# Kernel tuning notes

Hardware: AMD Instinct MI355X
Metric: run time of the kernel (lower is better)

The kernel has to match this reference:

```python
import jax, jax.numpy as jnp
import numpy as np

N_NODES = 100000
EPS = 1e-12  # F.normalize eps


def _sage_conv(x, src, dst, deg, Wl, bl, Wr):
    # mean aggregation of neighbor (source) features at destination nodes
    agg = jax.ops.segment_sum(x[src], dst, num_segments=N_NODES)  # [N, F]
    agg = agg / jnp.maximum(deg, 1.0)[:, None]
    out = agg @ Wl + bl + x @ Wr  # lin_l(mean(x_j)) + lin_r(x_i)
    # normalize=True -> L2 row normalization
    norm = jnp.sqrt(jnp.sum(out * out, axis=-1, keepdims=True))
    return out / jnp.maximum(norm, EPS)


def setup_inputs() -> dict:
    key = jax.random.key(0)
    ks = jax.random.split(key, 10)
    F_IN, H, C = 14, 32, 2
    x = jax.random.normal(ks[0], (N_NODES, F_IN), dtype=jnp.float32)
    edge_index = jax.random.randint(ks[1], (2, 6400000), 0, N_NODES, dtype=jnp.int32)
    def glorot(k, shape):
        lim = float(np.sqrt(6.0 / (shape[0] + shape[1])))
        return jax.random.uniform(k, shape, jnp.float32, -lim, lim)
    return {
        "x": x,
        "edge_index": edge_index,
        "W1l": glorot(ks[2], (F_IN, H)), "b1": jnp.zeros((H,), jnp.float32),
        "W1r": glorot(ks[3], (F_IN, H)),
        "W2l": glorot(ks[4], (H, H)), "b2": jnp.zeros((H,), jnp.float32),
        "W2r": glorot(ks[5], (H, H)),
        "Wlin": glorot(ks[6], (H, C)), "blin": jnp.zeros((C,), jnp.float32),
    }


def reference(x, edge_index, W1l, b1, W1r, W2l, b2, W2r, Wlin, blin):
    src, dst = edge_index[0], edge_index[1]
    deg = jax.ops.segment_sum(jnp.ones_like(dst, dtype=x.dtype), dst,
                              num_segments=N_NODES)  # in-degree per node
    h = jax.nn.relu(_sage_conv(x, src, dst, deg, W1l, b1, W1r))
    # dropout p=0.2 is identity at inference
    h = jax.nn.relu(_sage_conv(h, src, dst, deg, W2l, b2, W2r))
    return h @ Wlin + blin  # [N, num_classes]
```

## Files before the change

kernel.cpp:

```cpp
#include <hip/hip_runtime.h>
#include <hip/hip_bf16.h>


#define CHA 16384
#define MAXBH 800
#define CAPH 9728
#define NPB 128

static __device__ __forceinline__ unsigned short f2bf(float f) {
    unsigned u = __float_as_uint(f);
    unsigned r = (u + 0x7FFFu + ((u >> 16) & 1u)) >> 16;
    return (unsigned short)r;
}
#define BF_LO(u) __uint_as_float((u) << 16)
#define BF_HI(u) __uint_as_float((u) & 0xFFFF0000u)

__global__ void cvt_x_bf16(const float* __restrict__ x, unsigned short* __restrict__ xb,
                           int* __restrict__ bcursor, int N, int NBH) {
    int idx = blockIdx.x * blockDim.x + threadIdx.x;
    if (idx < NBH) bcursor[idx] = idx * CAPH;
    if (idx >= N * 16) return;
    int n = idx >> 4, f = idx & 15;
    float v = (f < 14) ? x[n * 14 + f] : 0.f;
    xb[idx] = f2bf(v);
}

__global__ __launch_bounds__(1024) void partitionA(
        const int* __restrict__ src, const int* __restrict__ dst,
        int* __restrict__ bcursor, unsigned* __restrict__ part, int E, int NBH) {
    __shared__ unsigned pk[CHA];
    __shared__ int h[MAXBH], lofs[MAXBH], delta[MAXBH];
    int t = threadIdx.x;
    int base = blockIdx.x * CHA;
    int end = base + CHA; if (end > E) end = E;
    int cnt = end - base;

    int ed[16], es[16], er[16];
    for (int i = t; i < NBH; i += 1024) h[i] = 0;
    __syncthreads();
    #pragma unroll
    for (int i = 0; i < 4; ++i) {
        int j = i * 4096 + t * 4;
        if (j + 4 <= cnt) {
            int4 d4 = *(const int4*)(dst + base + j);
            int4 s4 = *(const int4*)(src + base + j);
            ed[i*4+0] = d4.x; ed[i*4+1] = d4.y; ed[i*4+2] = d4.z; ed[i*4+3] = d4.w;
            es[i*4+0] = s4.x; es[i*4+1] = s4.y; es[i*4+2] = s4.z; es[i*4+3] = s4.w;
            er[i*4+0] = atomicAdd(&h[d4.x >> 7], 1);
            er[i*4+1] = atomicAdd(&h[d4.y >> 7], 1);
            er[i*4+2] = atomicAdd(&h[d4.z >> 7], 1);
            er[i*4+3] = atomicAdd(&h[d4.w >> 7], 1);
        } else {
            #pragma unroll
            for (int k = 0; k < 4; ++k) {
                if (j + k < cnt) {
                    ed[i*4+k] = dst[base + j + k];
                    es[i*4+k] = src[base + j + k];
                    er[i*4+k] = atomicAdd(&h[ed[i*4+k] >> 7], 1);
                } else ed[i*4+k] = -1;
            }
        }
    }
    __syncthreads();
    if (t < 64) {
        int vals[13];
        int run = 0;
        int b13 = t * 13;
        #pragma unroll
        for (int i = 0; i < 13; ++i) {
            int idx = b13 + i;
            int x = (idx < NBH) ? h[idx] : 0;
            run += x;
            vals[i] = run;
        }
        int tot = run, sc = run;
        #pragma unroll
        for (int off = 1; off < 64; off <<= 1) {
            int nv = __shfl_up(sc, off);
            if (t >= off) sc += nv;
        }
        int excl = sc - tot;
        #pragma unroll
        for (int i = 0; i < 13; ++i) {
            int idx = b13 + i;
            if (idx < NBH) {
                h[idx] = excl + vals[i];
                lofs[idx] = excl + (i ? vals[i - 1] : 0);
            }
        }
    }
    __syncthreads();
    if (t < NBH) {
        int excl = lofs[t];
        int v = h[t] - excl;
        int g = v ? atomicAdd(&bcursor[t], v) : 0;
        delta[t] = g - excl;
    }
    __syncthreads();
    #pragma unroll
    for (int i = 0; i < 16; ++i) {
        int d = ed[i];
        if (d >= 0) {
            int b = d >> 7;
            pk[lofs[b] + er[i]] = ((unsigned)(d & 127) << 24) | (unsigned)es[i];
        }
    }
    __syncthreads();
    int wid = t >> 6, lane = t & 63;
    for (int b = wid; b < NBH; b += 16) {
        int s = lofs[b];
        int e2 = h[b];
        int dlt = delta[b];
        int lim = (b + 1) * CAPH;
        for (int k = s + lane; k < e2; k += 64) {
            int gidx = dlt + k;
            if (gidx < lim) part[gidx] = pk[k];
        }
    }
}

__global__ __launch_bounds__(1024) void partitionB_fused(
        const unsigned* __restrict__ part, const int* __restrict__ bcursor,
        const uint4* __restrict__ xb4, const float* __restrict__ x,
        const float* __restrict__ W1l, const float* __restrict__ b1,
        const float* __restrict__ W1r,
        int* __restrict__ deg, int* __restrict__ offs, int* __restrict__ nlo,
        int* __restrict__ sorted_src, float* __restrict__ hbuf,
        unsigned short* __restrict__ hb, int N, int HALF) {
    __shared__ int pk2[CAPH];
    __shared__ int hh[256], keyofs[256];
    __shared__ int lstart[128], ldeg[128];
    __shared__ float sagg[128 * 17];
    __shared__ float sx[128 * 14];
    __shared__ float swl[448], swr[448], sb1[32];
    __shared__ int sTot;
    int hbid = blockIdx.x;
    int t = threadIdx.x;
    int start = hbid * CAPH;
    int end = bcursor[hbid];
    if (end > start + CAPH) end = start + CAPH;
    int cnt = end - start;
    unsigned ce[10];
    int rk[10];
    if (t < 256) hh[t] = 0;
    if (t >= 512 && t < 960) { swl[t - 512] = W1l[t - 512]; swr[t - 512] = W1r[t - 512]; }
    else if (t >= 960 && t < 992) sb1[t - 960] = b1[t - 960];
    __syncthreads();
    #pragma unroll
    for (int i = 0; i < 10; ++i) {
        int idx = start + t + i * 1024;
        unsigned p = 0xFFFFFFFFu;
        int r = 0;
        if (idx < end) {
            p = part[idx];
            int key = (int)(p >> 24) * 2 + (((int)(p & 0xFFFFFFu) < HALF) ? 0 : 1);
            r = atomicAdd(&hh[key], 1);
        }
        ce[i] = p;
        rk[i] = r;
    }
    {
        int nbase = hbid * 128;
        int nnod = N - nbase; if (nnod > 128) nnod = 128; if (nnod < 0) nnod = 0;
        const float* gx = x + (size_t)nbase * 14;
        for (int i = t; i < nnod * 14; i += 1024) sx[i] = gx[i];
    }
    __syncthreads();
    if (t < 64) {
        int b4 = t * 4;
        int v0 = hh[b4], v1 = hh[b4 + 1], v2 = hh[b4 + 2], v3 = hh[b4 + 3];
        int s1 = v0 + v1, s2 = s1 + v2, s3 = s2 + v3;
        int sc = s3;
        #pragma unroll
        for (int off = 1; off < 64; off <<= 1) {
            int nv = __shfl_up(sc, off);
            if (t >= off) sc += nv;
        }
        int excl = sc - s3;
        keyofs[b4]     = excl;
        keyofs[b4 + 1] = excl + v0;
        keyofs[b4 + 2] = excl + s1;
        keyofs[b4 + 3] = excl + s2;
        if (t == 63) sTot = excl + s3;
    }
    __syncthreads();
    if (t < 128) {
        int lo = hh[2 * t];
        int d = lo + hh[2 * t + 1];
        int excl = keyofs[2 * t];
        lstart[t] = excl;
        ldeg[t] = d;
        int node = hbid * 128 + t;
        if (node < N) {
            deg[node] = d;
            offs[node] = start + excl;
            nlo[node] = lo;
        }
    }
    __syncthreads();
    #pragma unroll
    for (int i = 0; i < 10; ++i) {
        unsigned p = ce[i];
        if (p != 0xFFFFFFFFu) {
            int s = (int)(p & 0xFFFFFFu);
            int key = (int)(p >> 24) * 2 + ((s < HALF) ? 0 : 1);
            int pos = keyofs[key] + rk[i];
            if (pos < CAPH) pk2[pos] = s;
        }
    }
    __syncthreads();
    int tot = sTot; if (tot > CAPH) tot = CAPH;
    for (int i = t; i < tot; i += 1024)
        sorted_src[start + i] = pk2[i];

    int node = t >> 3, sub = t & 7, ep = sub >> 1, half = sub & 1;
    int js = lstart[node], d = ldeg[node];
    int je = js + d;
    float a[8] = {0,0,0,0,0,0,0,0};
    int j = js + ep;
    for (; j + 12 < je; j += 16) {
        int s0 = pk2[j], s1 = pk2[j + 4], s2 = pk2[j + 8], s3 = pk2[j + 12];
        uint4 u0 = xb4[s0 * 2 + half], u1 = xb4[s1 * 2 + half];
        uint4 u2 = xb4[s2 * 2 + half], u3 = xb4[s3 * 2 + half];
        a[0] += (BF_LO(u0.x) + BF_LO(u1.x)) + (BF_LO(u2.x) + BF_LO(u3.x));
        a[1] += (BF_HI(u0.x) + BF_HI(u1.x)) + (BF_HI(u2.x) + BF_HI(u3.x));
        a[2] += (BF_LO(u0.y) + BF_LO(u1.y)) + (BF_LO(u2.y) + BF_LO(u3.y));
        a[3] += (BF_HI(u0.y) + BF_HI(u1.y)) + (BF_HI(u2.y) + BF_HI(u3.y));
        a[4] += (BF_LO(u0.z) + BF_LO(u1.z)) + (BF_LO(u2.z) + BF_LO(u3.z));
        a[5] += (BF_HI(u0.z) + BF_HI(u1.z)) + (BF_HI(u2.z) + BF_HI(u3.z));
        a[6] += (BF_LO(u0.w) + BF_LO(u1.w)) + (BF_LO(u2.w) + BF_LO(u3.w));
        a[7] += (BF_HI(u0.w) + BF_HI(u1.w)) + (BF_HI(u2.w) + BF_HI(u3.w));
    }
    for (; j + 4 < je; j += 8) {
        int s0 = pk2[j], s1 = pk2[j + 4];
        uint4 u0 = xb4[s0 * 2 + half], u1 = xb4[s1 * 2 + half];
        a[0] += BF_LO(u0.x) + BF_LO(u1.x);
        a[1] += BF_HI(u0.x) + BF_HI(u1.x);
        a[2] += BF_LO(u0.y) + BF_LO(u1.y);
        a[3] += BF_HI(u0.y) + BF_HI(u1.y);
        a[4] += BF_LO(u0.z) + BF_LO(u1.z);
        a[5] += BF_HI(u0.z) + BF_HI(u1.z);
        a[6] += BF_LO(u0.w) + BF_LO(u1.w);
        a[7] += BF_HI(u0.w) + BF_HI(u1.w);
    }
    for (; j < je; j += 4) {
        uint4 u0 = xb4[pk2[j] * 2 + half];
        a[0] += BF_LO(u0.x); a[1] += BF_HI(u0.x);
        a[2] += BF_LO(u0.y); a[3] += BF_HI(u0.y);
        a[4] += BF_LO(u0.z); a[5] += BF_HI(u0.z);
        a[6] += BF_LO(u0.w); a[7] += BF_HI(u0.w);
    }
    #pragma unroll
    for (int i = 0; i < 8; ++i) {
        a[i] += __shfl_xor(a[i], 2);
        a[i] += __shfl_xor(a[i], 4);
    }
    if (ep == 0) {
        #pragma unroll
        for (int i = 0; i < 8; ++i) sagg[node * 17 + half * 8 + i] = a[i];
    }
    __syncthreads();

    float inv = 1.0f / ((d > 0) ? (float)d : 1.0f);
    float acc[4];
    #pragma unroll
    for (int i = 0; i < 4; ++i) acc[i] = sb1[sub * 4 + i];
    #pragma unroll
    for (int k = 0; k < 14; ++k) {
        float ag = sagg[node * 17 + k] * inv;
        float xv = sx[node * 14 + k];
        float4 wl = *(const float4*)&swl[k * 32 + sub * 4];
        float4 wr = *(const float4*)&swr[k * 32 + sub * 4];
        acc[0] += ag * wl.x + xv * wr.x;
        acc[1] += ag * wl.y + xv * wr.y;
        acc[2] += ag * wl.z + xv * wr.z;
        acc[3] += ag * wl.w + xv * wr.w;
    }
    float ss = 0.f;
    #pragma unroll
    for (int i = 0; i < 4; ++i) ss += acc[i] * acc[i];
    ss += __shfl_xor(ss, 1); ss += __shfl_xor(ss, 2); ss += __shfl_xor(ss, 4);
    float invn = 1.f / fmaxf(sqrtf(ss), 1e-12f);
    int gnode = hbid * 128 + node;
    if (gnode < N) {
        float hv[4];
        #pragma unroll
        for (int i = 0; i < 4; ++i) hv[i] = fmaxf(acc[i] * invn, 0.f);
        *(float4*)(hbuf + (size_t)gnode * 32 + sub * 4) =
            make_float4(hv[0], hv[1], hv[2], hv[3]);
        uint2 pb;
        pb.x = (unsigned)f2bf(hv[0]) | ((unsigned)f2bf(hv[1]) << 16);
        pb.y = (unsigned)f2bf(hv[2]) | ((unsigned)f2bf(hv[3]) << 16);
        *(uint2*)(hb + (size_t)gnode * 32 + sub * 4) = pb;
    }
}

__global__ __launch_bounds__(256) void gather32_p0(
        const uint4* __restrict__ hb, const int* __restrict__ sorted_src,
        const int* __restrict__ offs, const int* __restrict__ nlo,
        float4* __restrict__ agg2a, int N) {
    int idx = blockIdx.x * blockDim.x + threadIdx.x;
    int n = idx >> 2;
    if (n >= N) return;
    int q = idx & 3;
    int start = offs[n];
    int jend = nlo[n];
    float a0=0,a1=0,a2=0,a3=0,a4=0,a5=0,a6=0,a7=0;
    int j = 0;
    for (; j + 8 <= jend; j += 8) {
        int s0 = sorted_src[start + j + 0];
        int s1 = sorted_src[start + j + 1];
        int s2 = sorted_src[start + j + 2];
        int s3 = sorted_src[start + j + 3];
        int s4 = sorted_src[start + j + 4];
        int s5 = sorted_src[start + j + 5];
        int s6 = sorted_src[start + j + 6];
        int s7 = sorted_src[start + j + 7];
        uint4 u0 = hb[s0 * 4 + q];
        uint4 u1 = hb[s1 * 4 + q];
        uint4 u2 = hb[s2 * 4 + q];
        uint4 u3 = hb[s3 * 4 + q];
        uint4 u4 = hb[s4 * 4 + q];
        uint4 u5 = hb[s5 * 4 + q];
        uint4 u6 = hb[s6 * 4 + q];
        uint4 u7 = hb[s7 * 4 + q];
        a0 += (BF_LO(u0.x)+BF_LO(u1.x)+BF_LO(u2.x)+BF_LO(u3.x))
            + (BF_LO(u4.x)+BF_LO(u5.x)+BF_LO(u6.x)+BF_LO(u7.x));
        a1 += (BF_HI(u0.x)+BF_HI(u1.x)+BF_HI(u2.x)+BF_HI(u3.x))
            + (BF_HI(u4.x)+BF_HI(u5.x)+BF_HI(u6.x)+BF_HI(u7.x));
        a2 += (BF_LO(u0.y)+BF_LO(u1.y)+BF_LO(u2.y)+BF_LO(u3.y))
            + (BF_LO(u4.y)+BF_LO(u5.y)+BF_LO(u6.y)+BF_LO(u7.y));
        a3 += (BF_HI(u0.y)+BF_HI(u1.y)+BF_HI(u2.y)+BF_HI(u3.y))
            + (BF_HI(u4.y)+BF_HI(u5.y)+BF_HI(u6.y)+BF_HI(u7.y));
        a4 += (BF_LO(u0.z)+BF_LO(u1.z)+BF_LO(u2.z)+BF_LO(u3.z))
            + (BF_LO(u4.z)+BF_LO(u5.z)+BF_LO(u6.z)+BF_LO(u7.z));
        a5 += (BF_HI(u0.z)+BF_HI(u1.z)+BF_HI(u2.z)+BF_HI(u3.z))
            + (BF_HI(u4.z)+BF_HI(u5.z)+BF_HI(u6.z)+BF_HI(u7.z));
        a6 += (BF_LO(u0.w)+BF_LO(u1.w)+BF_LO(u2.w)+BF_LO(u3.w))
            + (BF_LO(u4.w)+BF_LO(u5.w)+BF_LO(u6.w)+BF_LO(u7.w));
        a7 += (BF_HI(u0.w)+BF_HI(u1.w)+BF_HI(u2.w)+BF_HI(u3.w))
            + (BF_HI(u4.w)+BF_HI(u5.w)+BF_HI(u6.w)+BF_HI(u7.w));
    }
    for (; j + 4 <= jend; j += 4) {
        int s0 = sorted_src[start + j + 0];
        int s1 = sorted_src[start + j + 1];
        int s2 = sorted_src[start + j + 2];
        int s3 = sorted_src[start + j + 3];
        uint4 u0 = hb[s0 * 4 + q];
        uint4 u1 = hb[s1 * 4 + q];
        uint4 u2 = hb[s2 * 4 + q];
        uint4 u3 = hb[s3 * 4 + q];
        a0 += BF_LO(u0.x)+BF_LO(u1.x)+BF_LO(u2.x)+BF_LO(u3.x);
        a1 += BF_HI(u0.x)+BF_HI(u1.x)+BF_HI(u2.x)+BF_HI(u3.x);
        a2 += BF_LO(u0.y)+BF_LO(u1.y)+BF_LO(u2.y)+BF_LO(u3.y);
        a3 += BF_HI(u0.y)+BF_HI(u1.y)+BF_HI(u2.y)+BF_HI(u3.y);
        a4 += BF_LO(u0.z)+BF_LO(u1.z)+BF_LO(u2.z)+BF_LO(u3.z);
        a5 += BF_HI(u0.z)+BF_HI(u1.z)+BF_HI(u2.z)+BF_HI(u3.z);
        a6 += BF_LO(u0.w)+BF_LO(u1.w)+BF_LO(u2.w)+BF_LO(u3.w);
        a7 += BF_HI(u0.w)+BF_HI(u1.w)+BF_HI(u2.w)+BF_HI(u3.w);
    }
    for (; j < jend; ++j) {
        uint4 u0 = hb[sorted_src[start + j] * 4 + q];
        a0 += BF_LO(u0.x); a1 += BF_HI(u0.x);
        a2 += BF_LO(u0.y); a3 += BF_HI(u0.y);
        a4 += BF_LO(u0.z); a5 += BF_HI(u0.z);
        a6 += BF_LO(u0.w); a7 += BF_HI(u0.w);
    }
    agg2a[n * 8 + q * 2 + 0] = make_float4(a0, a1, a2, a3);
    agg2a[n * 8 + q * 2 + 1] = make_float4(a4, a5, a6, a7);
}

__global__ __launch_bounds__(256) void gather32_p1(
        const uint4* __restrict__ hb, const int* __restrict__ sorted_src,
        const int* __restrict__ offs, const int* __restrict__ deg,
        const int* __restrict__ nlo, float4* __restrict__ agg2b, int N) {
    int idx = blockIdx.x * blockDim.x + threadIdx.x;
    int n = idx >> 2;
    if (n >= N) return;
    int q = idx & 3;
    int start = offs[n];
    int d = deg[n];
    int j = nlo[n];
    float a0=0,a1=0,a2=0,a3=0,a4=0,a5=0,a6=0,a7=0;
    for (; j + 8 <= d; j += 8) {
        int s0 = sorted_src[start + j + 0];
        int s1 = sorted_src[start + j + 1];
        int s2 = sorted_src[start + j + 2];
        int s3 = sorted_src[start + j + 3];
        int s4 = sorted_src[start + j + 4];
        int s5 = sorted_src[start + j + 5];
        int s6 = sorted_src[start + j + 6];
        int s7 = sorted_src[start + j + 7];
        uint4 u0 = hb[s0 * 4 + q];
        uint4 u1 = hb[s1 * 4 + q];
        uint4 u2 = hb[s2 * 4 + q];
        uint4 u3 = hb[s3 * 4 + q];
        uint4 u4 = hb[s4 * 4 + q];
        uint4 u5 = hb[s5 * 4 + q];
        uint4 u6 = hb[s6 * 4 + q];
        uint4 u7 = hb[s7 * 4 + q];
        a0 += (BF_LO(u0.x)+BF_LO(u1.x)+BF_LO(u2.x)+BF_LO(u3.x))
            + (BF_LO(u4.x)+BF_LO(u5.x)+BF_LO(u6.x)+BF_LO(u7.x));
        a1 += (BF_HI(u0.x)+BF_HI(u1.x)+BF_HI(u2.x)+BF_HI(u3.x))
            + (BF_HI(u4.x)+BF_HI(u5.x)+BF_HI(u6.x)+BF_HI(u7.x));
        a2 += (BF_LO(u0.y)+BF_LO(u1.y)+BF_LO(u2.y)+BF_LO(u3.y))
            + (BF_LO(u4.y)+BF_LO(u5.y)+BF_LO(u6.y)+BF_LO(u7.y));
        a3 += (BF_HI(u0.y)+BF_HI(u1.y)+BF_HI(u2.y)+BF_HI(u3.y))
            + (BF_HI(u4.y)+BF_HI(u5.y)+BF_HI(u6.y)+BF_HI(u7.y));
        a4 += (BF_LO(u0.z)+BF_LO(u1.z)+BF_LO(u2.z)+BF_LO(u3.z))
            + (BF_LO(u4.z)+BF_LO(u5.z)+BF_LO(u6.z)+BF_LO(u7.z));
        a5 += (BF_HI(u0.z)+BF_HI(u1.z)+BF_HI(u2.z)+BF_HI(u3.z))
            + (BF_HI(u4.z)+BF_HI(u5.z)+BF_HI(u6.z)+BF_HI(u7.z));
        a6 += (BF_LO(u0.w)+BF_LO(u1.w)+BF_LO(u2.w)+BF_LO(u3.w))
            + (BF_LO(u4.w)+BF_LO(u5.w)+BF_LO(u6.w)+BF_LO(u7.w));
        a7 += (BF_HI(u0.w)+BF_HI(u1.w)+BF_HI(u2.w)+BF_HI(u3.w))
            + (BF_HI(u4.w)+BF_HI(u5.w)+BF_HI(u6.w)+BF_HI(u7.w));
    }
    for (; j + 4 <= d; j += 4) {
        int s0 = sorted_src[start + j + 0];
        int s1 = sorted_src[start + j + 1];
        int s2 = sorted_src[start + j + 2];
        int s3 = sorted_src[start + j + 3];
        uint4 u0 = hb[s0 * 4 + q];
        uint4 u1 = hb[s1 * 4 + q];
        uint4 u2 = hb[s2 * 4 + q];
        uint4 u3 = hb[s3 * 4 + q];
        a0 += BF_LO(u0.x)+BF_LO(u1.x)+BF_LO(u2.x)+BF_LO(u3.x);
        a1 += BF_HI(u0.x)+BF_HI(u1.x)+BF_HI(u2.x)+BF_HI(u3.x);
        a2 += BF_LO(u0.y)+BF_LO(u1.y)+BF_LO(u2.y)+BF_LO(u3.y);
        a3 += BF_HI(u0.y)+BF_HI(u1.y)+BF_HI(u2.y)+BF_HI(u3.y);
        a4 += BF_LO(u0.z)+BF_LO(u1.z)+BF_LO(u2.z)+BF_LO(u3.z);
        a5 += BF_HI(u0.z)+BF_HI(u1.z)+BF_HI(u2.z)+BF_HI(u3.z);
        a6 += BF_LO(u0.w)+BF_LO(u1.w)+BF_LO(u2.w)+BF_LO(u3.w);
        a7 += BF_HI(u0.w)+BF_HI(u1.w)+BF_HI(u2.w)+BF_HI(u3.w);
    }
    for (; j < d; ++j) {
        uint4 u0 = hb[sorted_src[start + j] * 4 + q];
        a0 += BF_LO(u0.x); a1 += BF_HI(u0.x);
        a2 += BF_LO(u0.y); a3 += BF_HI(u0.y);
        a4 += BF_LO(u0.z); a5 += BF_HI(u0.z);
        a6 += BF_LO(u0.w); a7 += BF_HI(u0.w);
    }
    agg2b[n * 8 + q * 2 + 0] = make_float4(a0, a1, a2, a3);
    agg2b[n * 8 + q * 2 + 1] = make_float4(a4, a5, a6, a7);
}

__global__ __launch_bounds__(256) void dense2(
        const float* __restrict__ h, const float* __restrict__ agg2a,
        const float* __restrict__ agg2b, const int* __restrict__ deg,
        const float* __restrict__ W2l, const float* __restrict__ b2,
        const float* __restrict__ W2r, const float* __restrict__ Wlin,
        const float* __restrict__ blin, float* __restrict__ out, int N) {
    __shared__ float sa[NPB * 33];
    __shared__ float sh2[NPB * 33];
    __shared__ float swl[32 * 32], swr[32 * 32], swo[64], sb[32], sbo[2];
    int t = threadIdx.x;
    int nb = blockIdx.x * NPB;
    int nn = N - nb; if (nn > NPB) nn = NPB;
    const float4* ga = (const float4*)(agg2a + (size_t)nb * 32);
    const float4* gb = (const float4*)(agg2b + (size_t)nb * 32);
    const float4* gh = (const float4*)(h + (size_t)nb * 32);
    for (int i = t; i < nn * 8; i += 256) {
        int row = i >> 3;
        int dv = deg[nb + row];
        float inv = 1.0f / ((dv > 0) ? (float)dv : 1.0f);
        float4 va = ga[i], vb = gb[i];
        float* d = &sa[row * 33 + (i & 7) * 4];
        d[0] = (va.x + vb.x) * inv; d[1] = (va.y + vb.y) * inv;
        d[2] = (va.z + vb.z) * inv; d[3] = (va.w + vb.w) * inv;
        float4 w = gh[i];
        float* e = &sh2[row * 33 + (i & 7) * 4];
        e[0] = w.x; e[1] = w.y; e[2] = w.z; e[3] = w.w;
    }
    for (int i = t; i < 1024; i += 256) { swl[i] = W2l[i]; swr[i] = W2r[i]; }
    if (t < 64) swo[t] = Wlin[t];
    if (t < 32) sb[t] = b2[t];
    if (t < 2) sbo[t] = blin[t];
    __syncthreads();
    int q2 = t & 3;
    int p = t >> 2;
    int l0 = p * 2, l1 = l0 + 1;
    float acc0[8], acc1[8];
    #pragma unroll
    for (int j = 0; j < 8; ++j) { acc0[j] = sb[q2 * 8 + j]; acc1[j] = acc0[j]; }
    for (int k = 0; k < 32; ++k) {
        float a0 = sa[l0 * 33 + k],  a1 = sa[l1 * 33 + k];
        float h0 = sh2[l0 * 33 + k], h1 = sh2[l1 * 33 + k];
        const float4* wl4 = (const float4*)&swl[k * 32 + q2 * 8];
        const float4* wr4 = (const float4*)&swr[k * 32 + q2 * 8];
        float4 wla = wl4[0], wlb = wl4[1], wra = wr4[0], wrb = wr4[1];
        acc0[0] += a0 * wla.x + h0 * wra.x;  acc1[0] += a1 * wla.x + h1 * wra.x;
        acc0[1] += a0 * wla.y + h0 * wra.y;  acc1[1] += a1 * wla.y + h1 * wra.y;
        acc0[2] += a0 * wla.z + h0 * wra.z;  acc1[2] += a1 * wla.z + h1 * wra.z;
        acc0[3] += a0 * wla.w + h0 * wra.w;  acc1[3] += a1 * wla.w + h1 * wra.w;
        acc0[4] += a0 * wlb.x + h0 * wrb.x;  acc1[4] += a1 * wlb.x + h1 * wrb.x;
        acc0[5] += a0 * wlb.y + h0 * wrb.y;  acc1[5] += a1 * wlb.y + h1 * wrb.y;
        acc0[6] += a0 * wlb.z + h0 * wrb.z;  acc1[6] += a1 * wlb.z + h1 * wrb.z;
        acc0[7] += a0 * wlb.w + h0 * wrb.w;  acc1[7] += a1 * wlb.w + h1 * wrb.w;
    }
    float ss0 = 0.f, ss1 = 0.f;
    #pragma unroll
    for (int j = 0; j < 8; ++j) { ss0 += acc0[j] * acc0[j]; ss1 += acc1[j] * acc1[j]; }
    ss0 += __shfl_xor(ss0, 1); ss0 += __shfl_xor(ss0, 2);
    ss1 += __shfl_xor(ss1, 1); ss1 += __shfl_xor(ss1, 2);
    float inv0 = 1.f / fmaxf(sqrtf(ss0), 1e-12f);
    float inv1 = 1.f / fmaxf(sqrtf(ss1), 1e-12f);
    float o00 = 0.f, o01 = 0.f, o10 = 0.f, o11 = 0.f;
    #pragma unroll
    for (int j = 0; j < 8; ++j) {
        float hv0 = fmaxf(acc0[j] * inv0, 0.f);
        float hv1 = fmaxf(acc1[j] * inv1, 0.f);
        int kk = q2 * 8 + j;
        o00 += hv0 * swo[kk * 2 + 0];
        o01 += hv0 * swo[kk * 2 + 1];
        o10 += hv1 * swo[kk * 2 + 0];
        o11 += hv1 * swo[kk * 2 + 1];
    }
    o00 += __shfl_xor(o00, 1); o00 += __shfl_xor(o00, 2);
    o01 += __shfl_xor(o01, 1); o01 += __shfl_xor(o01, 2);
    o10 += __shfl_xor(o10, 1); o10 += __shfl_xor(o10, 2);
    o11 += __shfl_xor(o11, 1); o11 += __shfl_xor(o11, 2);
    if (q2 == 0) {
        int n0 = nb + l0, n1 = nb + l1;
        if (n0 < N) { out[n0 * 2 + 0] = o00 + sbo[0]; out[n0 * 2 + 1] = o01 + sbo[1]; }
        if (n1 < N) { out[n1 * 2 + 0] = o10 + sbo[0]; out[n1 * 2 + 1] = o11 + sbo[1]; }
    }
}

extern "C" void kernel_launch(void* const* d_in, const int* in_sizes, int n_in,
                              void* d_out, int out_size, void* d_ws, size_t ws_size,
                              hipStream_t stream) {
    const float* x    = (const float*)d_in[0];
    const int*   ei   = (const int*)d_in[1];
    const float* W1l  = (const float*)d_in[2];
    const float* b1   = (const float*)d_in[3];
    const float* W1r  = (const float*)d_in[4];
    const float* W2l  = (const float*)d_in[5];
    const float* b2   = (const float*)d_in[6];
    const float* W2r  = (const float*)d_in[7];
    const float* Wlin = (const float*)d_in[8];
    const float* blin = (const float*)d_in[9];
    float* out = (float*)d_out;

    const int N = in_sizes[0] / 14;
    const int E = in_sizes[1] / 2;
    const int* src = ei;
    const int* dst = ei + E;
    const int NBH = (N + 127) / 128;
    const int HALF = N / 2;

    char* ws = (char*)d_ws;
    size_t off = 0;
    auto alloc = [&](size_t bytes) -> void* {
        void* p = ws + off;
        off = (off + bytes + 255) & ~(size_t)255;
        return p;
    };
    int*            bcursor    = (int*)alloc((size_t)NBH * 4);
    unsigned*       part       = (unsigned*)alloc((size_t)NBH * CAPH * 4);
    int*            sorted_src = (int*)alloc((size_t)NBH * CAPH * 4);
    int*            deg        = (int*)alloc((size_t)N * 4);
    int*            offs       = (int*)alloc((size_t)N * 4);
    int*            nlo        = (int*)alloc((size_t)N * 4);
    unsigned short* xb         = (unsigned short*)alloc((size_t)N * 16 * 2);
    float*          hbuf       = (float*)alloc((size_t)N * 32 * 4);
    unsigned short* hb         = (unsigned short*)alloc((size_t)N * 32 * 2);
    float*          agg2b      = (float*)alloc((size_t)N * 32 * 4);
    float*          agg2a      = (float*)part;
    (void)ws_size; (void)n_in; (void)out_size;

    cvt_x_bf16<<<(N * 16 + 255) / 256, 256, 0, stream>>>(x, xb, bcursor, N, NBH);
    partitionA<<<(E + CHA - 1) / CHA, 1024, 0, stream>>>(src, dst, bcursor, part, E, NBH);
    partitionB_fused<<<NBH, 1024, 0, stream>>>(
        part, bcursor, (const uint4*)xb, x, W1l, b1, W1r,
        deg, offs, nlo, sorted_src, hbuf, hb, N, HALF);
    gather32_p0<<<(N * 4 + 255) / 256, 256, 0, stream>>>(
        (const uint4*)hb, sorted_src, offs, nlo, (float4*)agg2a, N);
    gather32_p1<<<(N * 4 + 255) / 256, 256, 0, stream>>>(
        (const uint4*)hb, sorted_src, offs, deg, nlo, (float4*)agg2b, N);
    dense2<<<(N + NPB - 1) / NPB, 256, 0, stream>>>(
        hbuf, agg2a, agg2b, deg, W2l, b2, W2r, Wlin, blin, out, N);
}
```

Measured before the change: 274.1 us.

## Split fused partition-sort/layer-1 kernel into sort kernel and separate gather-dense kernel

Splits the large partitionB kernel: one kernel now only sorts edges by destination and writes sorted_src, degrees and offsets. A new 256-thread kernel then does the layer-1 neighbor gather from global sorted_src, using wave shuffles instead of shared-memory staging for the aggregate and x values. The aim is to free shared memory and allow more, smaller blocks for the latency-bound gather, rather than 782 heavy 1024-thread blocks. The cost is an extra launch and a re-read of sorted_src from global memory instead of LDS.

```diff
diff --git a/kernel.cpp b/kernel.cpp
--- a/kernel.cpp
+++ b/kernel.cpp
@@ -119,32 +119,21 @@
     }
 }
 
-__global__ __launch_bounds__(1024) void partitionB_fused(
+__global__ __launch_bounds__(1024) void partitionB_sort(
         const unsigned* __restrict__ part, const int* __restrict__ bcursor,
-        const uint4* __restrict__ xb4, const float* __restrict__ x,
-        const float* __restrict__ W1l, const float* __restrict__ b1,
-        const float* __restrict__ W1r,
         int* __restrict__ deg, int* __restrict__ offs, int* __restrict__ nlo,
-        int* __restrict__ sorted_src, float* __restrict__ hbuf,
-        unsigned short* __restrict__ hb, int N, int HALF) {
+        int* __restrict__ sorted_src, int N, int HALF) {
     __shared__ int pk2[CAPH];
     __shared__ int hh[256], keyofs[256];
-    __shared__ int lstart[128], ldeg[128];
-    __shared__ float sagg[128 * 17];
-    __shared__ float sx[128 * 14];
-    __shared__ float swl[448], swr[448], sb1[32];
     __shared__ int sTot;
     int hbid = blockIdx.x;
     int t = threadIdx.x;
     int start = hbid * CAPH;
     int end = bcursor[hbid];
     if (end > start + CAPH) end = start + CAPH;
-    int cnt = end - start;
     unsigned ce[10];
     int rk[10];
     if (t < 256) hh[t] = 0;
-    if (t >= 512 && t < 960) { swl[t - 512] = W1l[t - 512]; swr[t - 512] = W1r[t - 512]; }
-    else if (t >= 960 && t < 992) sb1[t - 960] = b1[t - 960];
     __syncthreads();
     #pragma unroll
     for (int i = 0; i < 10; ++i) {
@@ -158,12 +147,6 @@
         }
         ce[i] = p;
         rk[i] = r;
-    }
-    {
-        int nbase = hbid * 128;
-        int nnod = N - nbase; if (nnod > 128) nnod = 128; if (nnod < 0) nnod = 0;
-        const float* gx = x + (size_t)nbase * 14;
-        for (int i = t; i < nnod * 14; i += 1024) sx[i] = gx[i];
     }
     __syncthreads();
     if (t < 64) {
@@ -188,8 +171,6 @@
         int lo = hh[2 * t];
         int d = lo + hh[2 * t + 1];
         int excl = keyofs[2 * t];
-        lstart[t] = excl;
-        ldeg[t] = d;
         int node = hbid * 128 + t;
         if (node < N) {
             deg[node] = d;
@@ -197,7 +178,6 @@
             nlo[node] = lo;
         }
     }
-    __syncthreads();
     #pragma unroll
     for (int i = 0; i < 10; ++i) {
         unsigned p = ce[i];
@@ -212,14 +192,39 @@
     int tot = sTot; if (tot > CAPH) tot = CAPH;
     for (int i = t; i < tot; i += 1024)
         sorted_src[start + i] = pk2[i];
-
-    int node = t >> 3, sub = t & 7, ep = sub >> 1, half = sub & 1;
-    int js = lstart[node], d = ldeg[node];
+}
+
+__global__ __launch_bounds__(256) void gather14_dense1(
+        const uint4* __restrict__ xb4, const float* __restrict__ x,
+        const int* __restrict__ sorted_src, const int* __restrict__ offs,
+        const int* __restrict__ deg,
+        const float* __restrict__ W1l, const float* __restrict__ b1,
+        const float* __restrict__ W1r,
+        float* __restrict__ hbuf, unsigned short* __restrict__ hb, int N) {
+    __shared__ float swl[448], swr[448], sb1[32];
+    int t = threadIdx.x;
+    for (int i = t; i < 448; i += 256) { swl[i] = W1l[i]; swr[i] = W1r[i]; }
+    if (t < 32) sb1[t] = b1[t];
+    __syncthreads();
+
+    int node = blockIdx.x * 32 + (t >> 3);
+    int sub = t & 7, ep = sub >> 1, half = sub & 1;
+    int lanebase = (t & 63) & ~7;
+    bool valid = node < N;
+    int js = valid ? offs[node] : 0;
+    int d  = valid ? deg[node] : 0;
     int je = js + d;
+    float x0 = 0.f, x1 = 0.f;
+    if (valid && sub < 7) {
+        x0 = x[node * 14 + sub * 2];
+        x1 = x[node * 14 + sub * 2 + 1];
+    }
+
     float a[8] = {0,0,0,0,0,0,0,0};
     int j = js + ep;
     for (; j + 12 < je; j += 16) {
-        int s0 = pk2[j], s1 = pk2[j + 4], s2 = pk2[j + 8], s3 = pk2[j + 12];
+        int s0 = sorted_src[j], s1 = sorted_src[j + 4];
+        int s2 = sorted_src[j + 8], s3 = sorted_src[j + 12];
         uint4 u0 = xb4[s0 * 2 + half], u1 = xb4[s1 * 2 + half];
         uint4 u2 = xb4[s2 * 2 + half], u3 = xb4[s3 * 2 + half];
         a[0] += (BF_LO(u0.x) + BF_LO(u1.x)) + (BF_LO(u2.x) + BF_LO(u3.x));
@@ -232,7 +237,7 @@
         a[7] += (BF_HI(u0.w) + BF_HI(u1.w)) + (BF_HI(u2.w) + BF_HI(u3.w));
     }
     for (; j + 4 < je; j += 8) {
-        int s0 = pk2[j], s1 = pk2[j + 4];
+        int s0 = sorted_src[j], s1 = sorted_src[j + 4];
         uint4 u0 = xb4[s0 * 2 + half], u1 = xb4[s1 * 2 + half];
         a[0] += BF_LO(u0.x) + BF_LO(u1.x);
         a[1] += BF_HI(u0.x) + BF_HI(u1.x);
@@ -244,7 +249,7 @@
         a[7] += BF_HI(u0.w) + BF_HI(u1.w);
     }
     for (; j < je; j += 4) {
-        uint4 u0 = xb4[pk2[j] * 2 + half];
+        uint4 u0 = xb4[sorted_src[j] * 2 + half];
         a[0] += BF_LO(u0.x); a[1] += BF_HI(u0.x);
         a[2] += BF_LO(u0.y); a[3] += BF_HI(u0.y);
         a[4] += BF_LO(u0.z); a[5] += BF_HI(u0.z);
@@ -255,11 +260,6 @@
         a[i] += __shfl_xor(a[i], 2);
         a[i] += __shfl_xor(a[i], 4);
     }
-    if (ep == 0) {
-        #pragma unroll
-        for (int i = 0; i < 8; ++i) sagg[node * 17 + half * 8 + i] = a[i];
-    }
-    __syncthreads();
 
     float inv = 1.0f / ((d > 0) ? (float)d : 1.0f);
     float acc[4];
@@ -267,8 +267,8 @@
     for (int i = 0; i < 4; ++i) acc[i] = sb1[sub * 4 + i];
     #pragma unroll
     for (int k = 0; k < 14; ++k) {
-        float ag = sagg[node * 17 + k] * inv;
-        float xv = sx[node * 14 + k];
+        float ag = __shfl(a[k & 7], lanebase + (k >> 3)) * inv;
+        float xv = __shfl((k & 1) ? x1 : x0, lanebase + (k >> 1));
         float4 wl = *(const float4*)&swl[k * 32 + sub * 4];
         float4 wr = *(const float4*)&swr[k * 32 + sub * 4];
         acc[0] += ag * wl.x + xv * wr.x;
@@ -281,17 +281,16 @@
     for (int i = 0; i < 4; ++i) ss += acc[i] * acc[i];
     ss += __shfl_xor(ss, 1); ss += __shfl_xor(ss, 2); ss += __shfl_xor(ss, 4);
     float invn = 1.f / fmaxf(sqrtf(ss), 1e-12f);
-    int gnode = hbid * 128 + node;
-    if (gnode < N) {
+    if (valid) {
         float hv[4];
         #pragma unroll
         for (int i = 0; i < 4; ++i) hv[i] = fmaxf(acc[i] * invn, 0.f);
-        *(float4*)(hbuf + (size_t)gnode * 32 + sub * 4) =
+        *(float4*)(hbuf + (size_t)node * 32 + sub * 4) =
             make_float4(hv[0], hv[1], hv[2], hv[3]);
         uint2 pb;
         pb.x = (unsigned)f2bf(hv[0]) | ((unsigned)f2bf(hv[1]) << 16);
         pb.y = (unsigned)f2bf(hv[2]) | ((unsigned)f2bf(hv[3]) << 16);
-        *(uint2*)(hb + (size_t)gnode * 32 + sub * 4) = pb;
+        *(uint2*)(hb + (size_t)node * 32 + sub * 4) = pb;
     }
 }
 
@@ -569,11 +568,14 @@
     float*          agg2a      = (float*)part;
     (void)ws_size; (void)n_in; (void)out_size;
 
+    const int NB32 = (N + 31) / 32;
+
     cvt_x_bf16<<<(N * 16 + 255) / 256, 256, 0, stream>>>(x, xb, bcursor, N, NBH);
     partitionA<<<(E + CHA - 1) / CHA, 1024, 0, stream>>>(src, dst, bcursor, part, E, NBH);
-    partitionB_fused<<<NBH, 1024, 0, stream>>>(
-        part, bcursor, (const uint4*)xb, x, W1l, b1, W1r,
-        deg, offs, nlo, sorted_src, hbuf, hb, N, HALF);
+    partitionB_sort<<<NBH, 1024, 0, stream>>>(
+        part, bcursor, deg, offs, nlo, sorted_src, N, HALF);
+    gather14_dense1<<<NB32, 256, 0, stream>>>(
+        (const uint4*)xb, x, sorted_src, offs, deg, W1l, b1, W1r, hbuf, hb, N);
     gather32_p0<<<(N * 4 + 255) / 256, 256, 0, stream>>>(
         (const uint4*)hb, sorted_src, offs, nlo, (float4*)agg2a, N);
     gather32_p1<<<(N * 4 + 255) / 256, 256, 0, stream>>>(
```

Result: no change. 276.3 us (+0.8%).
